# Kernel tuning notes

Hardware: AMD Instinct MI355X
Metric: run time of the kernel (lower is better)

## Reference

```python
import jax, jax.numpy as jnp
import numpy as np

# --- dims (match init_kwargs) ---
B, S, D = 2, 2048, 2048
H, KV, HD = 16, 8, 128          # n_heads, n_kv_heads, head_dim = D // H
HID = 8192                      # 256 * ceil(4.0 * 2048 / 256)
COND = 1024                     # min(dim, 1024) adaLN input width
EPS = 1e-5                      # norm_eps for block RMSNorms
QK_EPS = 1.1920929e-07          # torch RMSNorm default eps=None -> finfo(fp32).eps


def rms(x, w, eps):
    return x * jax.lax.rsqrt(jnp.mean(jnp.square(x), axis=-1, keepdims=True) + eps) * w


def apply_rope(x, fc):
    # x: [b,s,h,d]; fc: [s,1,d//2,2,2] (2x2 rotation per freq)
    b, s, h, d = x.shape
    t = x.reshape(b, s, h, d // 2, 1, 2)
    out = fc[..., 0] * t[..., 0] + fc[..., 1] * t[..., 1]  # [b,s,h,d//2,2]
    return out.reshape(b, s, h, d)


def setup_inputs() -> dict:
    key = jax.random.key(0)
    ks = jax.random.split(key, 12)
    w = lambda k, shape: jax.random.normal(k, shape, jnp.float32) * 0.02

    x = jax.random.normal(ks[0], (B, S, D), jnp.float32)
    x_mask = jnp.ones((B, S), dtype=bool)  # accepted but unused (mask=None in attention)
    adaln_input = jax.random.normal(ks[1], (B, COND), jnp.float32)

    # proper RoPE rotation matrices: out0 = cos*x0 - sin*x1, out1 = sin*x0 + cos*x1
    pos = jnp.arange(S, dtype=jnp.float32)
    inv_freq = 10000.0 ** (-jnp.arange(0, HD, 2, dtype=jnp.float32) / HD)
    ang = pos[:, None] * inv_freq[None, :]            # [S, HD//2]
    cos, sin = jnp.cos(ang), jnp.sin(ang)
    freqs_cis = jnp.stack(
        [jnp.stack([cos, -sin], axis=-1), jnp.stack([sin, cos], axis=-1)], axis=-2
    )[:, None]                                        # [S,1,HD//2,2,2]

    return {
        "x": x,
        "x_mask": x_mask,
        "freqs_cis": freqs_cis,
        "adaln_input": adaln_input,
        "mod_w": w(ks[2], (4 * D, COND)),
        "mod_b": w(ks[3], (4 * D,)),
        "qkv_w": w(ks[4], ((H + 2 * KV) * HD, D)),
        "out_w": w(ks[5], (D, D)),
        "q_norm_w": jnp.ones((HD,), jnp.float32),
        "k_norm_w": jnp.ones((HD,), jnp.float32),
        "attn_norm1_w": jnp.ones((D,), jnp.float32),
        "attn_norm2_w": jnp.ones((D,), jnp.float32),
        "ffn_norm1_w": jnp.ones((D,), jnp.float32),
        "ffn_norm2_w": jnp.ones((D,), jnp.float32),
        "w1": w(ks[6], (HID, D)),
        "w2": w(ks[7], (D, HID)),
        "w3": w(ks[8], (HID, D)),
    }


def reference(x, x_mask, freqs_cis, adaln_input, mod_w, mod_b, qkv_w, out_w,
              q_norm_w, k_norm_w, attn_norm1_w, attn_norm2_w,
              ffn_norm1_w, ffn_norm2_w, w1, w2, w3):
    b, s, d = x.shape

    # adaLN modulation: SiLU -> Linear -> chunk(4)
    mod = jax.nn.silu(adaln_input) @ mod_w.T + mod_b        # [b, 4d]
    scale_msa, gate_msa, scale_mlp, gate_mlp = jnp.split(mod, 4, axis=1)

    # --- attention branch ---
    h = rms(x, attn_norm1_w, EPS) * (1.0 + scale_msa)[:, None, :]
    qkv = h @ qkv_w.T
    q, k, v = jnp.split(qkv, [H * HD, (H + KV) * HD], axis=-1)
    q = q.reshape(b, s, H, HD)
    k = k.reshape(b, s, KV, HD)
    v = v.reshape(b, s, KV, HD)
    q = apply_rope(rms(q, q_norm_w, QK_EPS), freqs_cis)
    k = apply_rope(rms(k, k_norm_w, QK_EPS), freqs_cis)
    n_rep = H // KV
    k = jnp.repeat(k, n_rep, axis=2)                        # [b,s,H,HD]
    v = jnp.repeat(v, n_rep, axis=2)
    scores = jnp.einsum('bqhd,bkhd->bhqk', q, k) / np.sqrt(HD).astype(np.float32)
    attn = jax.nn.softmax(scores, axis=-1)
    o = jnp.einsum('bhqk,bkhd->bqhd', attn, v).reshape(b, s, H * HD)
    o = o @ out_w.T
    x = x + jnp.tanh(gate_msa)[:, None, :] * rms(o, attn_norm2_w, EPS)

    # --- FFN branch (SwiGLU) ---
    h = rms(x, ffn_norm1_w, EPS) * (1.0 + scale_mlp)[:, None, :]
    ff = (jax.nn.silu(h @ w1.T) * (h @ w3.T)) @ w2.T
    x = x + jnp.tanh(gate_mlp)[:, None, :] * rms(ff, ffn_norm2_w, EPS)
    return x
```

## Files before the change

### kernel.cpp

```cpp
#include <hip/hip_runtime.h>

typedef __bf16 bf16_t;
typedef __bf16 bf16x8 __attribute__((ext_vector_type(8)));
typedef __bf16 bf16x4 __attribute__((ext_vector_type(4)));
typedef __bf16 bf16x2 __attribute__((ext_vector_type(2)));
typedef float f32x4 __attribute__((ext_vector_type(4)));

#define DEV __device__ __forceinline__

DEV void gload_lds16(const void* g, void* l) {
  __builtin_amdgcn_global_load_lds(
      (const __attribute__((address_space(1))) void*)g,
      (__attribute__((address_space(3))) void*)l, 16, 0, 0);
}

DEV float block_sum256(float v) {
  __shared__ float red[4];
#pragma unroll
  for (int m = 1; m <= 32; m <<= 1) v += __shfl_xor(v, m);
  __syncthreads();
  if ((threadIdx.x & 63) == 0) red[threadIdx.x >> 6] = v;
  __syncthreads();
  return red[0] + red[1] + red[2] + red[3];
}

template <int OUT_MODE>
__global__ __launch_bounds__(512, 2) void gemm_8p(const bf16_t* __restrict__ A,
                                                  const bf16_t* __restrict__ B,
                                                  void* __restrict__ Cv,
                                                  int M, int N, int Ks, int Klen) {
  constexpr int BM = 256;
  constexpr int MH = 4;
  constexpr int AU = 4;
  __shared__ bf16_t As[2 * BM * 64];
  __shared__ bf16_t Bs[2 * 256 * 64];

  const int tid = threadIdx.x;
  const int wave = tid >> 6, lane = tid & 63;
  const int wr = wave >> 2, wc = wave & 3;
  const int fr = lane & 15;
  const int z = blockIdx.y;
  A += (long)z * Klen;
  B += (long)z * Klen;

  int nwg = gridDim.x, wg = blockIdx.x;
  {
    int q = nwg >> 3, r = nwg & 7, xcd = wg & 7, loc = wg >> 3;
    wg = (xcd < r ? xcd * (q + 1) : r * (q + 1) + (xcd - r) * q) + loc;
  }
  const int ntn = N >> 8;
  const long row0 = (long)(wg / ntn) * BM;
  const long col0 = (long)(wg % ntn) << 8;

  const int srD = tid >> 3;
  const int scD = (tid & 7) << 4;
  const int skel = (scD ^ ((srD & 7) << 4)) >> 1;
  const long saoff = (row0 + srD) * (long)Ks + skel;
  const long sboff = (col0 + srD) * (long)Ks + skel;
  const int ldsu = wave << 9;

  const int nk = Klen >> 6;

  auto stageA = [&](int j, int u) {
    gload_lds16(A + saoff + (long)u * 64 * Ks + ((long)j << 6),
                As + ((j & 1) * BM * 64) + u * 4096 + ldsu);
  };
  auto stageB = [&](int j, int u) {
    gload_lds16(B + sboff + (long)u * 64 * Ks + ((long)j << 6),
                Bs + ((j & 1) * 256 * 64) + u * 4096 + ldsu);
  };
  const int fcb = (lane >> 4) << 4;
  auto frag = [&](const bf16_t* base, int r, int kk) -> bf16x8 {
    int c = (kk << 6) + fcb;
    c ^= (r & 7) << 4;
    return *(const bf16x8*)((const char*)base + r * 128 + c);
  };

#pragma unroll
  for (int u = 0; u < AU; ++u) stageA(0, u);
#pragma unroll
  for (int u = 0; u < 4; ++u) stageB(0, u);
#pragma unroll
  for (int u = 0; u < AU; ++u) stageA(1, u);
#pragma unroll
  for (int u = 0; u < 4; ++u) stageB(1, u);
  asm volatile("s_waitcnt vmcnt(8)" ::: "memory");
  __builtin_amdgcn_s_barrier();

  f32x4 acc[8][4] = {};
  bf16x8 af[MH][2], bfr[4][2];
  const int arow0 = wr * 128 + fr;
  const int brow0 = wc * 64 + fr;

  for (int j = 0; j < nk; ++j) {
    const bf16_t* Ab = As + (j & 1) * BM * 64;
    const bf16_t* Bb = Bs + (j & 1) * 256 * 64;
    const bool sA = (j >= 1) & (j + 1 < nk);
    const bool sB = (j + 2 < nk);

#pragma unroll
    for (int m = 0; m < MH; ++m)
#pragma unroll
      for (int kk = 0; kk < 2; ++kk) af[m][kk] = frag(Ab, arow0 + m * 16, kk);
#pragma unroll
    for (int n = 0; n < 2; ++n)
#pragma unroll
      for (int kk = 0; kk < 2; ++kk) bfr[n][kk] = frag(Bb, brow0 + n * 16, kk);
    if (sA) {
#pragma unroll
      for (int u = 0; u < AU / 2; ++u) stageA(j + 1, u);
    }
    __builtin_amdgcn_s_barrier();
    __builtin_amdgcn_s_setprio(1);
#pragma unroll
    for (int kk = 0; kk < 2; ++kk)
#pragma unroll
      for (int m = 0; m < MH; ++m)
#pragma unroll
        for (int n = 0; n < 2; ++n)
          acc[m][n] = __builtin_amdgcn_mfma_f32_16x16x32_bf16(
              af[m][kk], bfr[n][kk], acc[m][n], 0, 0, 0);
    __builtin_amdgcn_s_setprio(0);
    __builtin_amdgcn_s_barrier();

#pragma unroll
    for (int n = 2; n < 4; ++n)
#pragma unroll
      for (int kk = 0; kk < 2; ++kk) bfr[n][kk] = frag(Bb, brow0 + n * 16, kk);
    if (sA) {
#pragma unroll
      for (int u = AU / 2; u < AU; ++u) stageA(j + 1, u);
    }
    __builtin_amdgcn_s_barrier();
    __builtin_amdgcn_s_setprio(1);
#pragma unroll
    for (int kk = 0; kk < 2; ++kk)
#pragma unroll
      for (int m = 0; m < MH; ++m)
#pragma unroll
        for (int n = 2; n < 4; ++n)
          acc[m][n] = __builtin_amdgcn_mfma_f32_16x16x32_bf16(
              af[m][kk], bfr[n][kk], acc[m][n], 0, 0, 0);
    __builtin_amdgcn_s_setprio(0);
    __builtin_amdgcn_s_barrier();

#pragma unroll
    for (int m = 0; m < MH; ++m)
#pragma unroll
      for (int kk = 0; kk < 2; ++kk)
        af[m][kk] = frag(Ab, arow0 + (MH + m) * 16, kk);
    if (sB) {
      stageB(j + 2, 0);
      stageB(j + 2, 1);
    }
    __builtin_amdgcn_s_barrier();
    __builtin_amdgcn_s_setprio(1);
#pragma unroll
    for (int kk = 0; kk < 2; ++kk)
#pragma unroll
      for (int m = 0; m < MH; ++m)
#pragma unroll
        for (int n = 2; n < 4; ++n)
          acc[MH + m][n] = __builtin_amdgcn_mfma_f32_16x16x32_bf16(
              af[m][kk], bfr[n][kk], acc[MH + m][n], 0, 0, 0);
    __builtin_amdgcn_s_setprio(0);
    __builtin_amdgcn_s_barrier();

    if (sB) {
      stageB(j + 2, 2);
      stageB(j + 2, 3);
    }
    __builtin_amdgcn_s_barrier();
    __builtin_amdgcn_s_setprio(1);
#pragma unroll
    for (int kk = 0; kk < 2; ++kk)
#pragma unroll
      for (int m = 0; m < MH; ++m)
#pragma unroll
        for (int n = 0; n < 2; ++n)
          acc[MH + m][n] = __builtin_amdgcn_mfma_f32_16x16x32_bf16(
              af[m][kk], bfr[n][kk], acc[MH + m][n], 0, 0, 0);
    __builtin_amdgcn_s_setprio(0);
    asm volatile("s_waitcnt vmcnt(4)" ::: "memory");
    __builtin_amdgcn_s_barrier();
    __builtin_amdgcn_sched_barrier(0);
  }

  const int orow = wr * 128 + ((lane >> 4) << 2);
  const int ocol = wc * 64 + fr;
#pragma unroll
  for (int m = 0; m < 8; ++m)
#pragma unroll
    for (int n = 0; n < 4; ++n)
#pragma unroll
      for (int r = 0; r < 4; ++r) {
        long rr = row0 + orow + m * 16 + r;
        long cc = col0 + ocol + n * 16;
        if constexpr (OUT_MODE == 0) {
          ((float*)Cv)[(long)z * M * N + rr * N + cc] = acc[m][n][r];
        } else if constexpr (OUT_MODE == 1) {
          ((bf16_t*)Cv)[rr * N + cc] = (bf16_t)acc[m][n][r];
        } else {
          float g1v = acc[m][n][r];
          float g3v = __shfl_xor(g1v, 1);
          if (!(fr & 1)) {
            float s = g1v * g3v / (1.f + __expf(-g1v));
            ((bf16_t*)Cv)[rr * (N >> 1) + (cc >> 1)] = (bf16_t)s;
          }
        }
      }
}

__global__ __launch_bounds__(256) void adaln_mod(const float* __restrict__ adaln,
                                                 const float* __restrict__ mod_w,
                                                 const float* __restrict__ mod_b,
                                                 float* __restrict__ mod) {
  const int n = (blockIdx.x * 256 + threadIdx.x) >> 6;
  const int lane = threadIdx.x & 63;
  float a0 = 0.f, a1 = 0.f;
  const float* w = mod_w + (long)n * 1024;
  for (int c = lane; c < 1024; c += 64) {
    float wv = w[c];
    float x0 = adaln[c], x1 = adaln[1024 + c];
    a0 += wv * (x0 / (1.f + __expf(-x0)));
    a1 += wv * (x1 / (1.f + __expf(-x1)));
  }
#pragma unroll
  for (int m = 1; m <= 32; m <<= 1) {
    a0 += __shfl_xor(a0, m);
    a1 += __shfl_xor(a1, m);
  }
  if (lane == 0) {
    float bb = mod_b[n];
    mod[n] = a0 + bb;
    mod[8192 + n] = a1 + bb;
  }
}

__global__ __launch_bounds__(256) void norm_scale(const float* __restrict__ x,
                                                  const float* __restrict__ w,
                                                  const float* __restrict__ mod,
                                                  bf16_t* __restrict__ out) {
  const long row = blockIdx.x;
  const int b = (int)(row >> 11);
  const float* xr = x + row * 2048;
  float v[8];
  float ss = 0.f;
#pragma unroll
  for (int j = 0; j < 8; ++j) {
    v[j] = xr[threadIdx.x + (j << 8)];
    ss += v[j] * v[j];
  }
  ss = block_sum256(ss);
  float inv = rsqrtf(ss * (1.f / 2048.f) + 1e-5f);
  const float* sm = mod + b * 8192;
#pragma unroll
  for (int j = 0; j < 8; ++j) {
    int i = threadIdx.x + (j << 8);
    out[row * 2048 + i] = (bf16_t)(v[j] * inv * w[i] * (1.f + sm[i]));
  }
}

__global__ __launch_bounds__(256) void qknorm_rope(const bf16_t* __restrict__ qkv,
                                                   const float* __restrict__ fc,
                                                   const float* __restrict__ qw,
                                                   const float* __restrict__ kw,
                                                   bf16_t* __restrict__ qb,
                                                   bf16_t* __restrict__ kb) {
  const int gw = (blockIdx.x << 2) + (threadIdx.x >> 6);
  const int lane = threadIdx.x & 63;
  const int hh = gw % 24;
  const long tok = gw / 24;
  const int s = (int)(tok & 2047);
  const bf16_t* src = qkv + tok * 4096 + hh * 128 + lane * 2;
  float x0 = (float)src[0], x1 = (float)src[1];
  float ss = x0 * x0 + x1 * x1;
#pragma unroll
  for (int m = 1; m <= 32; m <<= 1) ss += __shfl_xor(ss, m);
  float inv = rsqrtf(ss * (1.f / 128.f) + 1.1920929e-07f);
  const float* w = (hh < 16) ? qw : kw;
  float n0 = x0 * inv * w[lane * 2], n1 = x1 * inv * w[lane * 2 + 1];
  float4 f = *(const float4*)(fc + ((long)s * 64 + lane) * 4);
  bf16x2 o;
  o[0] = (bf16_t)(f.x * n0 + f.y * n1);
  o[1] = (bf16_t)(f.z * n0 + f.w * n1);
  if (hh < 16)
    *(bf16x2*)(qb + (tok * 16 + hh) * 128 + lane * 2) = o;
  else
    *(bf16x2*)(kb + (tok * 8 + (hh - 16)) * 128 + lane * 2) = o;
}

__global__ __launch_bounds__(256) void vtrans(const bf16_t* __restrict__ qkv,
                                              bf16_t* __restrict__ vtb) {
  __shared__ bf16_t T[128 * 64];
  const int s0 = blockIdx.x << 6;
  const int bk = blockIdx.y;
  const int b = bk >> 3, kvh = bk & 7;
#pragma unroll
  for (int c = 0; c < 4; ++c) {
    int idx = threadIdx.x + (c << 8);
    int j = idx >> 4;
    int d0 = (idx & 15) << 3;
    bf16x8 v = *(const bf16x8*)(qkv + ((long)(b * 2048 + s0 + j)) * 4096 + 3072 +
                                kvh * 128 + d0);
#pragma unroll
    for (int e = 0; e < 8; ++e) {
      int row = d0 + e;
      int cb = (j << 1) ^ (((row >> 3) & 7) << 4);
      *(bf16_t*)((char*)T + (row << 7) + cb) = v[e];
    }
  }
  __syncthreads();
#pragma unroll
  for (int c = 0; c < 4; ++c) {
    int idx = threadIdx.x + (c << 8);
    int d = idx >> 3;
    int sb = (idx & 7) << 4;
    int cb = sb ^ (((d >> 3) & 7) << 4);
    bf16x8 v = *(const bf16x8*)((char*)T + (d << 7) + cb);
    *(bf16x8*)(vtb + ((long)bk * 128 + d) * 2048 + s0 + (sb >> 1)) = v;
  }
}

__global__ __launch_bounds__(512, 2) void attn_fwd(const bf16_t* __restrict__ Qb,
                                                   const bf16_t* __restrict__ Kb,
                                                   const bf16_t* __restrict__ Vt,
                                                   bf16_t* __restrict__ O) {
  const int S = 2048;
  __shared__ bf16_t Ks[2][64 * 128];
  __shared__ bf16_t Vs[2][128 * 64];
  __shared__ bf16_t Ps[8][32 * 64];

  const int tid = threadIdx.x, wave = tid >> 6, lane = tid & 63;
  const int qt = blockIdx.x, bh = blockIdx.y;
  const int b = bh >> 4, h = bh & 15;
  const int kvh = (bh & 15) >> 1;
  const int fr = lane & 15, fk = (lane >> 4) << 3;
  const float scale = 0.08838834764831845f;

  const long qrowA = (long)b * S + qt * 256 + wave * 32 + fr;
  bf16x8 qfA[4], qfB[4];
#pragma unroll
  for (int dc = 0; dc < 4; ++dc) {
    bf16x8 a = *(const bf16x8*)(Qb + qrowA * 2048 + h * 128 + (dc << 5) + fk);
    bf16x8 c = *(const bf16x8*)(Qb + (qrowA + 16) * 2048 + h * 128 + (dc << 5) + fk);
#pragma unroll
    for (int e = 0; e < 8; ++e) {
      a[e] = (bf16_t)((float)a[e] * scale);
      c[e] = (bf16_t)((float)c[e] * scale);
    }
    qfA[dc] = a;
    qfB[dc] = c;
  }

  auto stageK = [&](int kt, int bi) {
#pragma unroll
    for (int c = 0; c < 2; ++c) {
      int row = (c << 5) + (tid >> 4);
      int cb = ((tid & 15) << 4) ^ ((row & 7) << 4);
      gload_lds16(Kb + ((long)(b * S + (kt << 6) + row) * 8 + kvh) * 128 + (cb >> 1),
                  (char*)Ks[bi] + (c << 13) + (wave << 10));
    }
  };
  auto stageV = [&](int kt, int bi) {
#pragma unroll
    for (int c = 0; c < 2; ++c) {
      int row = (c << 6) + (tid >> 3);
      int cb = ((tid & 7) << 4) ^ ((row & 7) << 4);
      gload_lds16(Vt + ((long)(bh >> 1) * 128 + row) * 2048 + (kt << 6) + (cb >> 1),
                  (char*)Vs[bi] + (c << 13) + (wave << 10));
    }
  };

  stageK(0, 0);
  stageV(0, 0);

  f32x4 oA[8] = {}, oB[8] = {};
  float lpA[4] = {0.f, 0.f, 0.f, 0.f}, lpB[4] = {0.f, 0.f, 0.f, 0.f};
  const int prow = (lane >> 4) << 2;
  __syncthreads();

  for (int kt = 0; kt < 32; ++kt) {
    const int bi = kt & 1;
    if (kt + 1 < 32) {
      stageK(kt + 1, bi ^ 1);
      stageV(kt + 1, bi ^ 1);
    }

    const char* Kbuf = (const char*)Ks[bi];
    f32x4 scA[4], scB[4];
#pragma unroll
    for (int jt = 0; jt < 4; ++jt) {
      f32x4 zA = {}, zB = {};
#pragma unroll
      for (int dc = 0; dc < 4; ++dc) {
        int row = (jt << 4) + fr;
        int cb = ((dc << 6) + (fk << 1)) ^ ((row & 7) << 4);
        bf16x8 kf = *(const bf16x8*)(Kbuf + (row << 8) + cb);
        zA = __builtin_amdgcn_mfma_f32_16x16x32_bf16(qfA[dc], kf, zA, 0, 0, 0);
        zB = __builtin_amdgcn_mfma_f32_16x16x32_bf16(qfB[dc], kf, zB, 0, 0, 0);
      }
      scA[jt] = zA;
      scB[jt] = zB;
    }

    char* PsW = (char*)Ps[wave];
#pragma unroll
    for (int jt = 0; jt < 4; ++jt)
#pragma unroll
      for (int r = 0; r < 4; ++r) {
        float pA = __expf(scA[jt][r]);
        float pB = __expf(scB[jt][r]);
        lpA[r] += pA;
        lpB[r] += pB;
        int row = prow + r;
        int cb = (((jt << 4) + fr) << 1) ^ ((row & 7) << 4);
        *(bf16_t*)(PsW + (row << 7) + cb) = (bf16_t)pA;
        *(bf16_t*)(PsW + ((row + 16) << 7) + cb) = (bf16_t)pB;
      }

    const char* Vbuf = (const char*)Vs[bi];
#pragma unroll
    for (int kc = 0; kc < 2; ++kc) {
      int cbp = ((kc << 6) + (fk << 1)) ^ ((fr & 7) << 4);
      bf16x8 paA = *(const bf16x8*)(PsW + (fr << 7) + cbp);
      bf16x8 paB = *(const bf16x8*)(PsW + ((fr + 16) << 7) + cbp);
#pragma unroll
      for (int dt = 0; dt < 8; ++dt) {
        int row = (dt << 4) + fr;
        int cb = ((kc << 6) + (fk << 1)) ^ ((row & 7) << 4);
        bf16x8 vf = *(const bf16x8*)(Vbuf + (row << 7) + cb);
        oA[dt] = __builtin_amdgcn_mfma_f32_16x16x32_bf16(paA, vf, oA[dt], 0, 0, 0);
        oB[dt] = __builtin_amdgcn_mfma_f32_16x16x32_bf16(paB, vf, oB[dt], 0, 0, 0);
      }
    }
    __syncthreads();
  }

#pragma unroll
  for (int r = 0; r < 4; ++r) {
#pragma unroll
    for (int m = 1; m <= 8; m <<= 1) {
      lpA[r] += __shfl_xor(lpA[r], m);
      lpB[r] += __shfl_xor(lpB[r], m);
    }
    lpA[r] = 1.f / lpA[r];
    lpB[r] = 1.f / lpB[r];
  }
  const long orA = (long)b * S + qt * 256 + wave * 32 + prow;
#pragma unroll
  for (int dt = 0; dt < 8; ++dt)
#pragma unroll
    for (int r = 0; r < 4; ++r) {
      O[(orA + r) * 2048 + h * 128 + (dt << 4) + fr] = (bf16_t)(oA[dt][r] * lpA[r]);
      O[(orA + 16 + r) * 2048 + h * 128 + (dt << 4) + fr] =
          (bf16_t)(oB[dt][r] * lpB[r]);
    }
}

__global__ __launch_bounds__(256) void resid1(const float* __restrict__ x,
                                              const float* __restrict__ oproj,
                                              const float* __restrict__ mod,
                                              const float* __restrict__ n2w,
                                              const float* __restrict__ fn1w,
                                              float* __restrict__ x1,
                                              bf16_t* __restrict__ h2) {
  const long row = blockIdx.x;
  const int b = (int)(row >> 11);
  const float* op0 = oproj + row * 2048;
  const float* op1 = op0 + 8388608L;
  float ov[8];
  float ss = 0.f;
#pragma unroll
  for (int j = 0; j < 8; ++j) {
    int i = threadIdx.x + (j << 8);
    ov[j] = op0[i] + op1[i];
    ss += ov[j] * ov[j];
  }
  ss = block_sum256(ss);
  float inv = rsqrtf(ss * (1.f / 2048.f) + 1e-5f);
  const float* gmsa = mod + b * 8192 + 2048;
  const float* smlp = mod + b * 8192 + 4096;
  float xv[8];
  float ss2 = 0.f;
#pragma unroll
  for (int j = 0; j < 8; ++j) {
    int i = threadIdx.x + (j << 8);
    float xn = x[row * 2048 + i] + tanhf(gmsa[i]) * (ov[j] * inv * n2w[i]);
    xv[j] = xn;
    ss2 += xn * xn;
    x1[row * 2048 + i] = xn;
  }
  ss2 = block_sum256(ss2);
  float inv2 = rsqrtf(ss2 * (1.f / 2048.f) + 1e-5f);
#pragma unroll
  for (int j = 0; j < 8; ++j) {
    int i = threadIdx.x + (j << 8);
    h2[row * 2048 + i] = (bf16_t)(xv[j] * inv2 * fn1w[i] * (1.f + smlp[i]));
  }
}

__global__ __launch_bounds__(256) void resid2(const float* __restrict__ x1,
                                              const float* __restrict__ w2out,
                                              const float* __restrict__ mod,
                                              const float* __restrict__ fn2w,
                                              float* __restrict__ out) {
  const long row = blockIdx.x;
  const int b = (int)(row >> 11);
  const float* f0 = w2out + row * 2048;
  const float* f1 = f0 + 8388608L;
  float fv[8];
  float ss = 0.f;
#pragma unroll
  for (int j = 0; j < 8; ++j) {
    int i = threadIdx.x + (j << 8);
    fv[j] = f0[i] + f1[i];
    ss += fv[j] * fv[j];
  }
  ss = block_sum256(ss);
  float inv = rsqrtf(ss * (1.f / 2048.f) + 1e-5f);
  const float* gmlp = mod + b * 8192 + 6144;
#pragma unroll
  for (int j = 0; j < 8; ++j) {
    int i = threadIdx.x + (j << 8);
    out[row * 2048 + i] = x1[row * 2048 + i] + tanhf(gmlp[i]) * (fv[j] * inv * fn2w[i]);
  }
}

__global__ __launch_bounds__(256) void cast_f32_bf16(const float* __restrict__ in,
                                                     bf16_t* __restrict__ out, long n) {
  long i0 = ((long)blockIdx.x * 256 + threadIdx.x) << 2;
  long stride = (long)gridDim.x * 1024;
  for (long i = i0; i < n; i += stride) {
    float4 v = *(const float4*)(in + i);
    bf16x4 o;
    o[0] = (bf16_t)v.x;
    o[1] = (bf16_t)v.y;
    o[2] = (bf16_t)v.z;
    o[3] = (bf16_t)v.w;
    *(bf16x4*)(out + i) = o;
  }
}

__global__ __launch_bounds__(256) void cast_ilv(const float* __restrict__ a,
                                                const float* __restrict__ b,
                                                bf16_t* __restrict__ o) {
  const long n = 8192L * 2048;
  long i0 = ((long)blockIdx.x * 256 + threadIdx.x) << 3;
  long stride = (long)gridDim.x * 2048;
  for (long p = i0; p < n; p += stride) {
    long row = p >> 11;
    long col = p & 2047;
    float4 a0 = *(const float4*)(a + p), a1 = *(const float4*)(a + p + 4);
    float4 b0 = *(const float4*)(b + p), b1 = *(const float4*)(b + p + 4);
    bf16x8 oa, ob;
    oa[0] = (bf16_t)a0.x; oa[1] = (bf16_t)a0.y; oa[2] = (bf16_t)a0.z; oa[3] = (bf16_t)a0.w;
    oa[4] = (bf16_t)a1.x; oa[5] = (bf16_t)a1.y; oa[6] = (bf16_t)a1.z; oa[7] = (bf16_t)a1.w;
    ob[0] = (bf16_t)b0.x; ob[1] = (bf16_t)b0.y; ob[2] = (bf16_t)b0.z; ob[3] = (bf16_t)b0.w;
    ob[4] = (bf16_t)b1.x; ob[5] = (bf16_t)b1.y; ob[6] = (bf16_t)b1.z; ob[7] = (bf16_t)b1.w;
    *(bf16x8*)(o + (row << 12) + col) = oa;
    *(bf16x8*)(o + (row << 12) + 2048 + col) = ob;
  }
}

extern "C" void kernel_launch(void* const* d_in, const int* in_sizes, int n_in,
                              void* d_out, int out_size, void* d_ws, size_t ws_size,
                              hipStream_t stream) {
  (void)in_sizes; (void)n_in; (void)out_size; (void)ws_size;
  const float* x     = (const float*)d_in[0];
  const float* fc    = (const float*)d_in[2];
  const float* adaln = (const float*)d_in[3];
  const float* mod_w = (const float*)d_in[4];
  const float* mod_b = (const float*)d_in[5];
  const float* qkv_w = (const float*)d_in[6];
  const float* out_w = (const float*)d_in[7];
  const float* qnw   = (const float*)d_in[8];
  const float* knw   = (const float*)d_in[9];
  const float* n1w   = (const float*)d_in[10];
  const float* n2w   = (const float*)d_in[11];
  const float* fn1w  = (const float*)d_in[12];
  const float* fn2w  = (const float*)d_in[13];
  const float* w1    = (const float*)d_in[14];
  const float* w2    = (const float*)d_in[15];
  const float* w3    = (const float*)d_in[16];
  float* out = (float*)d_out;

  char* ws = (char*)d_ws;
  size_t off = 0;
  auto alloc = [&](size_t sz) {
    void* p = ws + off;
    off += (sz + 255) & ~(size_t)255;
    return p;
  };
  float*  MOD  = (float*)alloc(2L * 8192 * 4);
  bf16_t* WA   = (bf16_t*)alloc(4096L * 2048 * 2);
  bf16_t* W13B = (bf16_t*)alloc(16384L * 2048 * 2);
  bf16_t* W2B  = (bf16_t*)alloc(2048L * 8192 * 2);
  bf16_t* S1   = (bf16_t*)alloc(4096L * 2048 * 2);
  void*   S2   = alloc(4096L * 4096 * 4);
  void*   S3   = alloc(4096L * 4096 * 2);
  float*  S4   = (float*)alloc(2L * 4096 * 2048 * 4);

  bf16_t* qb  = (bf16_t*)S3;
  bf16_t* kb  = qb + 4096L * 2048;
  bf16_t* vtb = kb + 4096L * 1024;
  float* x1 = (float*)S3;

  adaln_mod<<<2048, 256, 0, stream>>>(adaln, mod_w, mod_b, MOD);
  norm_scale<<<4096, 256, 0, stream>>>(x, n1w, MOD, S1);
  cast_f32_bf16<<<2048, 256, 0, stream>>>(qkv_w, WA, 4096L * 2048);
  gemm_8p<1><<<dim3(256, 1), 512, 0, stream>>>(S1, WA, S2, 4096, 4096, 2048, 2048);
  qknorm_rope<<<24576, 256, 0, stream>>>((const bf16_t*)S2, fc, qnw, knw, qb, kb);
  vtrans<<<dim3(32, 16), 256, 0, stream>>>((const bf16_t*)S2, vtb);
  attn_fwd<<<dim3(8, 32), 512, 0, stream>>>(qb, kb, vtb, S1);
  cast_f32_bf16<<<2048, 256, 0, stream>>>(out_w, WA, 2048L * 2048);
  gemm_8p<0><<<dim3(128, 2), 512, 0, stream>>>(S1, WA, S4, 4096, 2048, 2048, 1024);
  resid1<<<4096, 256, 0, stream>>>(x, S4, MOD, n2w, fn1w, x1, S1);
  cast_ilv<<<2048, 256, 0, stream>>>(w1, w3, W13B);
  gemm_8p<2><<<dim3(1024, 1), 512, 0, stream>>>(S1, W13B, S2, 4096, 16384, 2048, 2048);
  cast_f32_bf16<<<2048, 256, 0, stream>>>(w2, W2B, 2048L * 8192);
  gemm_8p<0><<<dim3(128, 2), 512, 0, stream>>>((const bf16_t*)S2, W2B, S4, 4096, 2048,
                                               8192, 4096);
  resid2<<<4096, 256, 0, stream>>>(x1, S4, MOD, fn2w, out);
}
```

Baseline: 786.8 us.

## Switch GEMM to 32x32x16 MFMA tiles and column-per-XCD workgroup mapping

Replaces the 16x16x32 bf16 MFMA fragments with 32x32x16 MFMA, restructuring fragment loads, accumulator layout and the epilogue index mapping accordingly. This halves the MFMA instruction count and changes LDS read patterns per wave. It also adds a new workgroup-to-tile mapping that assigns contiguous column strips to each XCD when N allows, aiming to improve L2 locality of the B operand. Risks are higher register pressure from larger accumulators and possible LDS bank conflicts with the new fragment offsets.

```diff
diff --git a/kernel.cpp b/kernel.cpp
--- a/kernel.cpp
+++ b/kernel.cpp
@@ -5,6 +5,7 @@
 typedef __bf16 bf16x4 __attribute__((ext_vector_type(4)));
 typedef __bf16 bf16x2 __attribute__((ext_vector_type(2)));
 typedef float f32x4 __attribute__((ext_vector_type(4)));
+typedef float f32x16 __attribute__((ext_vector_type(16)));
 
 #define DEV __device__ __forceinline__
 
@@ -30,27 +31,32 @@
                                                   void* __restrict__ Cv,
                                                   int M, int N, int Ks, int Klen) {
   constexpr int BM = 256;
-  constexpr int MH = 4;
-  constexpr int AU = 4;
   __shared__ bf16_t As[2 * BM * 64];
   __shared__ bf16_t Bs[2 * 256 * 64];
 
   const int tid = threadIdx.x;
   const int wave = tid >> 6, lane = tid & 63;
   const int wr = wave >> 2, wc = wave & 3;
-  const int fr = lane & 15;
+  const int fr = lane & 31;
+  const int fh = lane >> 5;
   const int z = blockIdx.y;
   A += (long)z * Klen;
   B += (long)z * Klen;
 
+  const int ntn = N >> 8;
   int nwg = gridDim.x, wg = blockIdx.x;
-  {
+  long row0, col0;
+  if (((ntn & 7) == 0) && ((ntn >> 3) >= 4) && ((nwg & 7) == 0)) {
+    int cpx = ntn >> 3;
+    int xcd = wg & 7, loc = wg >> 3;
+    row0 = (long)(loc / cpx) * BM;
+    col0 = ((long)(xcd * cpx + loc % cpx)) << 8;
+  } else {
     int q = nwg >> 3, r = nwg & 7, xcd = wg & 7, loc = wg >> 3;
     wg = (xcd < r ? xcd * (q + 1) : r * (q + 1) + (xcd - r) * q) + loc;
-  }
-  const int ntn = N >> 8;
-  const long row0 = (long)(wg / ntn) * BM;
-  const long col0 = (long)(wg % ntn) << 8;
+    row0 = (long)(wg / ntn) * BM;
+    col0 = (long)(wg % ntn) << 8;
+  }
 
   const int srD = tid >> 3;
   const int scD = (tid & 7) << 4;
@@ -69,26 +75,25 @@
     gload_lds16(B + sboff + (long)u * 64 * Ks + ((long)j << 6),
                 Bs + ((j & 1) * 256 * 64) + u * 4096 + ldsu);
   };
-  const int fcb = (lane >> 4) << 4;
   auto frag = [&](const bf16_t* base, int r, int kk) -> bf16x8 {
-    int c = (kk << 6) + fcb;
+    int c = (kk << 5) + (fh << 4);
     c ^= (r & 7) << 4;
     return *(const bf16x8*)((const char*)base + r * 128 + c);
   };
 
 #pragma unroll
-  for (int u = 0; u < AU; ++u) stageA(0, u);
+  for (int u = 0; u < 4; ++u) stageA(0, u);
 #pragma unroll
   for (int u = 0; u < 4; ++u) stageB(0, u);
 #pragma unroll
-  for (int u = 0; u < AU; ++u) stageA(1, u);
+  for (int u = 0; u < 4; ++u) stageA(1, u);
 #pragma unroll
   for (int u = 0; u < 4; ++u) stageB(1, u);
   asm volatile("s_waitcnt vmcnt(8)" ::: "memory");
   __builtin_amdgcn_s_barrier();
 
-  f32x4 acc[8][4] = {};
-  bf16x8 af[MH][2], bfr[4][2];
+  f32x16 acc[4][2] = {};
+  bf16x8 af[2][4], bfr[2][4];
   const int arow0 = wr * 128 + fr;
   const int brow0 = wc * 64 + fr;
 
@@ -99,56 +104,47 @@
     const bool sB = (j + 2 < nk);
 
 #pragma unroll
-    for (int m = 0; m < MH; ++m)
-#pragma unroll
-      for (int kk = 0; kk < 2; ++kk) af[m][kk] = frag(Ab, arow0 + m * 16, kk);
-#pragma unroll
-    for (int n = 0; n < 2; ++n)
-#pragma unroll
-      for (int kk = 0; kk < 2; ++kk) bfr[n][kk] = frag(Bb, brow0 + n * 16, kk);
+    for (int m = 0; m < 2; ++m)
+#pragma unroll
+      for (int kk = 0; kk < 4; ++kk) af[m][kk] = frag(Ab, arow0 + m * 32, kk);
+#pragma unroll
+    for (int kk = 0; kk < 4; ++kk) bfr[0][kk] = frag(Bb, brow0, kk);
     if (sA) {
-#pragma unroll
-      for (int u = 0; u < AU / 2; ++u) stageA(j + 1, u);
+      stageA(j + 1, 0);
+      stageA(j + 1, 1);
     }
     __builtin_amdgcn_s_barrier();
     __builtin_amdgcn_s_setprio(1);
 #pragma unroll
-    for (int kk = 0; kk < 2; ++kk)
-#pragma unroll
-      for (int m = 0; m < MH; ++m)
-#pragma unroll
-        for (int n = 0; n < 2; ++n)
-          acc[m][n] = __builtin_amdgcn_mfma_f32_16x16x32_bf16(
-              af[m][kk], bfr[n][kk], acc[m][n], 0, 0, 0);
+    for (int kk = 0; kk < 4; ++kk)
+#pragma unroll
+      for (int m = 0; m < 2; ++m)
+        acc[m][0] = __builtin_amdgcn_mfma_f32_32x32x16_bf16(af[m][kk], bfr[0][kk],
+                                                            acc[m][0], 0, 0, 0);
     __builtin_amdgcn_s_setprio(0);
     __builtin_amdgcn_s_barrier();
 
 #pragma unroll
-    for (int n = 2; n < 4; ++n)
-#pragma unroll
-      for (int kk = 0; kk < 2; ++kk) bfr[n][kk] = frag(Bb, brow0 + n * 16, kk);
+    for (int kk = 0; kk < 4; ++kk) bfr[1][kk] = frag(Bb, brow0 + 32, kk);
     if (sA) {
-#pragma unroll
-      for (int u = AU / 2; u < AU; ++u) stageA(j + 1, u);
+      stageA(j + 1, 2);
+      stageA(j + 1, 3);
     }
     __builtin_amdgcn_s_barrier();
     __builtin_amdgcn_s_setprio(1);
 #pragma unroll
-    for (int kk = 0; kk < 2; ++kk)
-#pragma unroll
-      for (int m = 0; m < MH; ++m)
-#pragma unroll
-        for (int n = 2; n < 4; ++n)
-          acc[m][n] = __builtin_amdgcn_mfma_f32_16x16x32_bf16(
-              af[m][kk], bfr[n][kk], acc[m][n], 0, 0, 0);
+    for (int kk = 0; kk < 4; ++kk)
+#pragma unroll
+      for (int m = 0; m < 2; ++m)
+        acc[m][1] = __builtin_amdgcn_mfma_f32_32x32x16_bf16(af[m][kk], bfr[1][kk],
+                                                            acc[m][1], 0, 0, 0);
     __builtin_amdgcn_s_setprio(0);
     __builtin_amdgcn_s_barrier();
 
 #pragma unroll
-    for (int m = 0; m < MH; ++m)
-#pragma unroll
-      for (int kk = 0; kk < 2; ++kk)
-        af[m][kk] = frag(Ab, arow0 + (MH + m) * 16, kk);
+    for (int m = 0; m < 2; ++m)
+#pragma unroll
+      for (int kk = 0; kk < 4; ++kk) af[m][kk] = frag(Ab, arow0 + (2 + m) * 32, kk);
     if (sB) {
       stageB(j + 2, 0);
       stageB(j + 2, 1);
@@ -156,13 +152,11 @@
     __builtin_amdgcn_s_barrier();
     __builtin_amdgcn_s_setprio(1);
 #pragma unroll
-    for (int kk = 0; kk < 2; ++kk)
-#pragma unroll
-      for (int m = 0; m < MH; ++m)
-#pragma unroll
-        for (int n = 2; n < 4; ++n)
-          acc[MH + m][n] = __builtin_amdgcn_mfma_f32_16x16x32_bf16(
-              af[m][kk], bfr[n][kk], acc[MH + m][n], 0, 0, 0);
+    for (int kk = 0; kk < 4; ++kk)
+#pragma unroll
+      for (int m = 0; m < 2; ++m)
+        acc[2 + m][1] = __builtin_amdgcn_mfma_f32_32x32x16_bf16(af[m][kk], bfr[1][kk],
+                                                                acc[2 + m][1], 0, 0, 0);
     __builtin_amdgcn_s_setprio(0);
     __builtin_amdgcn_s_barrier();
 
@@ -173,38 +167,36 @@
     __builtin_amdgcn_s_barrier();
     __builtin_amdgcn_s_setprio(1);
 #pragma unroll
-    for (int kk = 0; kk < 2; ++kk)
-#pragma unroll
-      for (int m = 0; m < MH; ++m)
-#pragma unroll
-        for (int n = 0; n < 2; ++n)
-          acc[MH + m][n] = __builtin_amdgcn_mfma_f32_16x16x32_bf16(
-              af[m][kk], bfr[n][kk], acc[MH + m][n], 0, 0, 0);
+    for (int kk = 0; kk < 4; ++kk)
+#pragma unroll
+      for (int m = 0; m < 2; ++m)
+        acc[2 + m][0] = __builtin_amdgcn_mfma_f32_32x32x16_bf16(af[m][kk], bfr[0][kk],
+                                                                acc[2 + m][0], 0, 0, 0);
     __builtin_amdgcn_s_setprio(0);
     asm volatile("s_waitcnt vmcnt(4)" ::: "memory");
     __builtin_amdgcn_s_barrier();
     __builtin_amdgcn_sched_barrier(0);
   }
 
-  const int orow = wr * 128 + ((lane >> 4) << 2);
   const int ocol = wc * 64 + fr;
-#pragma unroll
-  for (int m = 0; m < 8; ++m)
-#pragma unroll
-    for (int n = 0; n < 4; ++n)
-#pragma unroll
-      for (int r = 0; r < 4; ++r) {
-        long rr = row0 + orow + m * 16 + r;
-        long cc = col0 + ocol + n * 16;
+  const int orow0 = wr * 128 + (fh << 2);
+#pragma unroll
+  for (int mt = 0; mt < 4; ++mt)
+#pragma unroll
+    for (int nt = 0; nt < 2; ++nt)
+#pragma unroll
+      for (int g = 0; g < 16; ++g) {
+        long rr = row0 + orow0 + mt * 32 + (g & 3) + ((g >> 2) << 3);
+        long cc = col0 + ocol + nt * 32;
+        float v = acc[mt][nt][g];
         if constexpr (OUT_MODE == 0) {
-          ((float*)Cv)[(long)z * M * N + rr * N + cc] = acc[m][n][r];
+          ((float*)Cv)[(long)z * M * N + rr * N + cc] = v;
         } else if constexpr (OUT_MODE == 1) {
-          ((bf16_t*)Cv)[rr * N + cc] = (bf16_t)acc[m][n][r];
+          ((bf16_t*)Cv)[rr * N + cc] = (bf16_t)v;
         } else {
-          float g1v = acc[m][n][r];
-          float g3v = __shfl_xor(g1v, 1);
-          if (!(fr & 1)) {
-            float s = g1v * g3v / (1.f + __expf(-g1v));
+          float g3v = __shfl_xor(v, 1);
+          if (!(lane & 1)) {
+            float s = v * g3v / (1.f + __expf(-v));
             ((bf16_t*)Cv)[rr * (N >> 1) + (cc >> 1)] = (bf16_t)s;
           }
         }
```

Measured after the change: 820.0 us. 4.2% more time.
